# Kernel tuning notes

Measured on AMD Instinct MI355X. Metric: run time of the kernel, lower is better.

Reference implementation:

```python
import jax, jax.numpy as jnp
import numpy as np

D_MODEL = 2048
NUM_HEADS = 16
NUM_KV_HEADS = 4
HEAD_DIM = D_MODEL // NUM_HEADS  # 128
ROPE_THETA = 10000.0
BATCH = 2
SEQ = 2048


def _rotate_half(x):
    # interleaved rotate-half: pairs (x0,x1) -> (-x1, x0)
    x1 = x[..., ::2]
    x2 = x[..., 1::2]
    return jnp.stack((-x2, x1), axis=-1).reshape(x.shape)


def _rope_tables(seq_len, dtype, start_pos=0):
    inv_freq = 1.0 / (ROPE_THETA ** (jnp.arange(0, HEAD_DIM, 2, dtype=jnp.float32) / HEAD_DIM))
    positions = jnp.arange(start_pos, start_pos + seq_len, dtype=jnp.float32)
    freqs = jnp.outer(positions, inv_freq)              # [S, HD/2]
    emb = jnp.repeat(freqs, 2, axis=-1)                  # [S, HD]
    cos = jnp.cos(emb).astype(dtype)[None, None, :, :]   # [1,1,S,HD]
    sin = jnp.sin(emb).astype(dtype)[None, None, :, :]
    return cos, sin


def setup_inputs() -> dict:
    key = jax.random.key(0)
    ks = jax.random.split(key, 5)
    s = 0.02
    x = jax.random.normal(ks[0], (BATCH, SEQ, D_MODEL), dtype=jnp.float32)
    wq = jax.random.normal(ks[1], (D_MODEL, NUM_HEADS * HEAD_DIM), dtype=jnp.float32) * s
    wk = jax.random.normal(ks[2], (D_MODEL, NUM_KV_HEADS * HEAD_DIM), dtype=jnp.float32) * s
    wv = jax.random.normal(ks[3], (D_MODEL, NUM_KV_HEADS * HEAD_DIM), dtype=jnp.float32) * s
    wo = jax.random.normal(ks[4], (D_MODEL, D_MODEL), dtype=jnp.float32) * s
    return {"x": x, "wq": wq, "wk": wk, "wv": wv, "wo": wo}


def reference(x, wq, wk, wv, wo):
    batch, seq_len, _ = x.shape
    # projections (bias-free linears)
    q = (x @ wq).reshape(batch, seq_len, NUM_HEADS, HEAD_DIM).transpose(0, 2, 1, 3)
    k = (x @ wk).reshape(batch, seq_len, NUM_KV_HEADS, HEAD_DIM).transpose(0, 2, 1, 3)
    v = (x @ wv).reshape(batch, seq_len, NUM_KV_HEADS, HEAD_DIM).transpose(0, 2, 1, 3)
    # RoPE
    cos, sin = _rope_tables(seq_len, q.dtype)
    q = q * cos + _rotate_half(q) * sin
    k = k * cos + _rotate_half(k) * sin
    # GQA: duplicate KV heads
    repeats = NUM_HEADS // NUM_KV_HEADS
    k = jnp.repeat(k, repeats, axis=1)
    v = jnp.repeat(v, repeats, axis=1)
    # causal SDPA
    scale = HEAD_DIM ** -0.5
    scores = jnp.einsum('bhqd,bhkd->bhqk', q, k) * scale
    causal = jnp.tril(jnp.ones((seq_len, seq_len), dtype=bool))
    scores = jnp.where(causal[None, None, :, :], scores, -jnp.inf)
    weights = jax.nn.softmax(scores, axis=-1)
    y = jnp.einsum('bhqk,bhkd->bhqd', weights, v)
    y = y.transpose(0, 2, 1, 3).reshape(batch, seq_len, NUM_HEADS * HEAD_DIM)
    return y @ wo
```

## Files before the change

### kernel.cpp

```cpp
#include <hip/hip_runtime.h>
#include <cstdint>
#include <cstddef>

using short8 = __attribute__((ext_vector_type(8))) short;
using f32x4  = __attribute__((ext_vector_type(4))) float;
using u16x4  = __attribute__((ext_vector_type(4))) unsigned short;

#define DEV __device__ __forceinline__

DEV unsigned short f2bf(float f) {
  unsigned int u = __builtin_bit_cast(unsigned int, f);
  u += 0x7fffu + ((u >> 16) & 1u);
  return (unsigned short)(u >> 16);
}
DEV float bf2f(unsigned short h) {
  unsigned int u = ((unsigned int)h) << 16;
  return __builtin_bit_cast(float, u);
}
DEV unsigned int cvtpk_bf16(float lo, float hi) {
  unsigned int d;
  asm("v_cvt_pk_bf16_f32 %0, %1, %2" : "=v"(d) : "v"(lo), "v"(hi));
  return d;
}

#define GLL16(gp, lp)                                                          \
  __builtin_amdgcn_global_load_lds(                                            \
      (const __attribute__((address_space(1))) char*)(const char*)(gp),        \
      (__attribute__((address_space(3))) char*)(char*)(lp), 16, 0, 0)

constexpr int BATCH = 2, SEQ = 2048, DMODEL = 2048, NH = 16, NKVH = 4, DH = 128;
constexpr int MROWS = BATCH * SEQ;
constexpr int NQKV  = DMODEL + 2 * NKVH * DH;
constexpr int KOFF  = DMODEL;
constexpr int VOFF  = DMODEL + NKVH * DH;
constexpr float SM_L2 = 0.12751388158f;


__global__ void k_tables(float* __restrict__ tc, float* __restrict__ ts) {
  int id = blockIdx.x * 256 + threadIdx.x;
  int pos = id >> 6, i = id & 63;
  float freq = __expf(-(float)i * 0.14391157f);
  float ang = (float)pos * freq;
  tc[id] = cosf(ang);
  ts[id] = sinf(ang);
}

__global__ void k_castx(const float* __restrict__ x, unsigned short* __restrict__ xb) {
  int id = blockIdx.x * 256 + threadIdx.x;
  float4 v = ((const float4*)x)[id];
  u16x4 o = { f2bf(v.x), f2bf(v.y), f2bf(v.z), f2bf(v.w) };
  ((u16x4*)xb)[id] = o;
}

__global__ __launch_bounds__(256) void k_wtrans(const float* __restrict__ src,
                                                unsigned short* __restrict__ dst, int N) {
  __shared__ float tile[32][33];
  int n0 = blockIdx.x * 32, k0 = blockIdx.y * 32;
  int tx = threadIdx.x, ty = threadIdx.y;
  #pragma unroll
  for (int r = ty; r < 32; r += 8)
    tile[r][tx] = src[(size_t)(k0 + r) * N + n0 + tx];
  __syncthreads();
  #pragma unroll
  for (int r = ty; r < 32; r += 8)
    dst[(size_t)(n0 + r) * 2048 + k0 + tx] = f2bf(tile[tx][r]);
}

__global__ __launch_bounds__(256) void k_vtrans(const unsigned short* __restrict__ qkv,
                                                unsigned short* __restrict__ vt) {
  __shared__ unsigned short tile[32][33];
  int s0 = blockIdx.x * 32, d0 = blockIdx.y * 32;
  int bk = blockIdx.z;
  const unsigned short* src = qkv + (size_t)(bk >> 2) * SEQ * NQKV + VOFF + (bk & 3) * DH;
  unsigned short* dst = vt + ((size_t)bk * DH + d0) * SEQ + s0;
  int tx = threadIdx.x, ty = threadIdx.y;
  #pragma unroll
  for (int r = ty; r < 32; r += 8)
    tile[r][tx] = src[(size_t)(s0 + r) * NQKV + d0 + tx];
  __syncthreads();
  #pragma unroll
  for (int r = ty; r < 32; r += 8)
    dst[(size_t)r * SEQ + tx] = tile[tx][r];
}


constexpr int BM = 128, BN = 128, BK = 32;

template <bool OUTF32>
__global__ __launch_bounds__(256) void k_gemm_bt(
    const unsigned short* __restrict__ A,
    const unsigned short* __restrict__ Bt,
    void* __restrict__ C, int M, int N, int K) {
  __shared__ unsigned short As[BM * BK];
  __shared__ unsigned short Bs[BN * BK];
  const int t = threadIdx.x;
  const int l = t & 63, w = t >> 6;
  const int wm = w >> 1, wn = w & 1;
  const int gx = gridDim.x;
  const int nwg = gx * gridDim.y;
  const int idl = blockIdx.y * gx + blockIdx.x;
  const int swz = (idl & 7) * (nwg >> 3) + (idl >> 3);
  const int m0 = (swz / gx) * BM, n0 = (swz % gx) * BN;
  const int rl = l & 15, kg = l >> 4;

  f32x4 acc[4][4] = {};

  const int sr = t >> 2;
  const int gq = (t & 3) ^ (sr & 3);
  const unsigned short* aP0 = A  + (size_t)(m0 + sr) * K + gq * 8;
  const unsigned short* aP1 = A  + (size_t)(m0 + 64 + sr) * K + gq * 8;
  const unsigned short* bP0 = Bt + (size_t)(n0 + sr) * K + gq * 8;
  const unsigned short* bP1 = Bt + (size_t)(n0 + 64 + sr) * K + gq * 8;
  char* ldsA = (char*)As;
  char* ldsB = (char*)Bs;
  const int wb = w * 1024;

  const int nk = K / BK;
  for (int kt = 0; kt < nk; ++kt) {
    const int ko = kt * BK;
    __syncthreads();
    GLL16(aP0 + ko, ldsA + wb);
    GLL16(aP1 + ko, ldsA + 4096 + wb);
    GLL16(bP0 + ko, ldsB + wb);
    GLL16(bP1 + ko, ldsB + 4096 + wb);
    __syncthreads();
    short8 aF[4], bF[4];
    #pragma unroll
    for (int mi = 0; mi < 4; ++mi) {
      int r = wm * 64 + mi * 16 + rl;
      aF[mi] = *(const short8*)(ldsA + r * 64 + ((kg ^ (r & 3)) * 16));
    }
    #pragma unroll
    for (int ni = 0; ni < 4; ++ni) {
      int r = wn * 64 + ni * 16 + rl;
      bF[ni] = *(const short8*)(ldsB + r * 64 + ((kg ^ (r & 3)) * 16));
    }
    #pragma unroll
    for (int mi = 0; mi < 4; ++mi)
      #pragma unroll
      for (int ni = 0; ni < 4; ++ni)
        acc[mi][ni] = __builtin_amdgcn_mfma_f32_16x16x32_bf16(aF[mi], bF[ni], acc[mi][ni], 0, 0, 0);
  }

  #pragma unroll
  for (int mi = 0; mi < 4; ++mi) {
    #pragma unroll
    for (int ni = 0; ni < 4; ++ni) {
      int row = m0 + wm * 64 + mi * 16 + kg * 4;
      int col = n0 + wn * 64 + ni * 16 + rl;
      #pragma unroll
      for (int r = 0; r < 4; ++r) {
        if constexpr (OUTF32)
          ((float*)C)[(size_t)(row + r) * N + col] = acc[mi][ni][r];
        else
          ((unsigned short*)C)[(size_t)(row + r) * N + col] = f2bf(acc[mi][ni][r]);
      }
    }
  }
}


__global__ void k_rope(unsigned short* __restrict__ qkv,
                       const float* __restrict__ tc, const float* __restrict__ ts) {
  int id = blockIdx.x * 256 + threadIdx.x;
  int row = id / 1280, p = id % 1280;
  int col, d;
  bool isq = (p < 1024);
  if (isq) { col = 2 * p;               d = p & 63; }
  else     { int pk = p - 1024; col = KOFF + 2 * pk; d = pk & 63; }
  int s = row & (SEQ - 1);
  float c = tc[s * 64 + d], sn = ts[s * 64 + d];
  unsigned int* pp = (unsigned int*)(qkv + (size_t)row * NQKV + col);
  unsigned int v = *pp;
  float x0 = bf2f((unsigned short)(v & 0xffffu));
  float x1 = bf2f((unsigned short)(v >> 16));
  float y0 = x0 * c - x1 * sn;
  float y1 = x1 * c + x0 * sn;
  if (isq) { y0 *= SM_L2; y1 *= SM_L2; }
  *pp = (unsigned int)f2bf(y0) | ((unsigned int)f2bf(y1) << 16);
}


constexpr int QB = 128, KB = 64;
constexpr float THR = 8.0f;

__global__ __launch_bounds__(512, 8) void k_attn(const unsigned short* __restrict__ qkv,
                                                 const unsigned short* __restrict__ vt,
                                                 unsigned short* __restrict__ obuf) {
  __shared__ unsigned short Ks[KB * DH];
  __shared__ unsigned short Vs[DH * KB];
  __shared__ unsigned short Pw[8][16 * 72];

  const int t = threadIdx.x, l = t & 63, w = t >> 6;
  const int rl = l & 15, kg = l >> 4;

  const int id = blockIdx.x;
  const int b = id >> 8;
  const int u = id & 255;
  const int h = u >> 4;
  const int qtr = u & 15;
  const int qt = b ? (15 - qtr) : qtr;
  const int q0 = qt * QB;
  const int kvh = h >> 2;

  const unsigned short* qbase = qkv + (size_t)b * SEQ * NQKV;
  const unsigned short* kbase = qbase + KOFF + kvh * DH;
  const unsigned short* vtb = vt + (size_t)(b * NKVH + kvh) * DH * SEQ;

  const unsigned short* kp[2];
  const unsigned short* vp[2];
  #pragma unroll
  for (int i = 0; i < 2; ++i) {
    int c = i * 512 + t;
    int krow = c >> 4, kq = c & 15;
    kp[i] = kbase + (size_t)krow * NQKV + ((kq ^ (krow & 7)) << 3);
    int vrow = c >> 3, vq = c & 7;
    vp[i] = vtb + (size_t)vrow * SEQ + ((vq ^ (vrow & 7)) << 3);
  }

  const int qw0 = q0 + w * 16;

  short8 qF[4];
  {
    const size_t qr = (size_t)(qw0 + rl) * NQKV + h * DH;
    #pragma unroll
    for (int ks = 0; ks < 4; ++ks)
      qF[ks] = *(const short8*)(qbase + qr + ks * 32 + kg * 8);
  }

  f32x4 Oc[8] = {};
  float mr = -3e38f, lr = 0.f;

  unsigned short* pw = Pw[w];

  for (int kv0 = 0; kv0 < q0 + QB; kv0 += KB) {
    __syncthreads();
    #pragma unroll
    for (int i = 0; i < 2; ++i) {
      GLL16(kp[i] + (size_t)kv0 * NQKV, (char*)Ks + w * 1024 + i * 8192);
      GLL16(vp[i] + kv0,               (char*)Vs + w * 1024 + i * 8192);
    }
    __syncthreads();
    if (kv0 >= qw0 + 16) continue;

    f32x4 St[4] = {};
    __builtin_amdgcn_s_setprio(1);
    #pragma unroll
    for (int n = 0; n < 4; ++n) {
      const int krow = n * 16 + rl;
      #pragma unroll
      for (int ks = 0; ks < 4; ++ks) {
        short8 kF = *(const short8*)&Ks[krow * DH + (((ks * 4 + kg) ^ (rl & 7)) << 3)];
        St[n] = __builtin_amdgcn_mfma_f32_16x16x32_bf16(kF, qF[ks], St[n], 0, 0, 0);
      }
    }
    __builtin_amdgcn_s_setprio(0);

    float mx = -3e38f;
    const bool diag = (kv0 + KB - 1) > qw0;
    if (diag) {
      const int thr = qw0 + rl - kv0;
      #pragma unroll
      for (int n = 0; n < 4; ++n)
        #pragma unroll
        for (int r = 0; r < 4; ++r) {
          float s = St[n][r];
          if (n * 16 + kg * 4 + r > thr) s = -3e38f;
          St[n][r] = s;
          mx = fmaxf(mx, s);
        }
    } else {
      #pragma unroll
      for (int n = 0; n < 4; ++n)
        #pragma unroll
        for (int r = 0; r < 4; ++r) mx = fmaxf(mx, St[n][r]);
    }
    mx = fmaxf(mx, __shfl_xor(mx, 16));
    mx = fmaxf(mx, __shfl_xor(mx, 32));

    const bool need = mx > mr + THR;
    if (__any(need)) {
      const float mnew = fmaxf(mr, mx);
      const float sf = exp2f(mr - mnew);
      mr = mnew;
      lr *= sf;
      float sfv[4];
      #pragma unroll
      for (int r = 0; r < 4; ++r) sfv[r] = __shfl(sf, kg * 4 + r, 16);
      #pragma unroll
      for (int c = 0; c < 8; ++c)
        #pragma unroll
        for (int r = 0; r < 4; ++r) Oc[c][r] *= sfv[r];
    }

    float rs = 0.f;
    #pragma unroll
    for (int n = 0; n < 4; ++n) {
      float e0 = exp2f(St[n][0] - mr);
      float e1 = exp2f(St[n][1] - mr);
      float e2 = exp2f(St[n][2] - mr);
      float e3 = exp2f(St[n][3] - mr);
      rs += (e0 + e1) + (e2 + e3);
      uint2 d;
      d.x = cvtpk_bf16(e0, e1);
      d.y = cvtpk_bf16(e2, e3);
      *(uint2*)&pw[rl * 72 + n * 16 + kg * 4] = d;
    }
    rs += __shfl_xor(rs, 16);
    rs += __shfl_xor(rs, 32);
    lr += rs;

    short8 pF[2];
    #pragma unroll
    for (int ks2 = 0; ks2 < 2; ++ks2)
      pF[ks2] = *(const short8*)&pw[rl * 72 + ks2 * 32 + kg * 8];
    __builtin_amdgcn_s_setprio(1);
    #pragma unroll
    for (int c = 0; c < 8; ++c) {
      const int vrow = c * 16 + rl;
      #pragma unroll
      for (int ks2 = 0; ks2 < 2; ++ks2) {
        short8 vF = *(const short8*)&Vs[vrow * KB + (((ks2 * 4 + kg) ^ (rl & 7)) << 3)];
        Oc[c] = __builtin_amdgcn_mfma_f32_16x16x32_bf16(pF[ks2], vF, Oc[c], 0, 0, 0);
      }
    }
    __builtin_amdgcn_s_setprio(0);
  }

  const float linv = 1.0f / lr;
  float inv[4];
  #pragma unroll
  for (int r = 0; r < 4; ++r) inv[r] = __shfl(linv, kg * 4 + r, 16);
  #pragma unroll
  for (int c = 0; c < 8; ++c)
    #pragma unroll
    for (int r = 0; r < 4; ++r) {
      int row = b * SEQ + qw0 + kg * 4 + r;
      obuf[(size_t)row * DMODEL + h * DH + c * 16 + rl] = f2bf(Oc[c][r] * inv[r]);
    }
}


extern "C" void kernel_launch(void* const* d_in, const int* in_sizes, int n_in,
                              void* d_out, int out_size, void* d_ws, size_t ws_size,
                              hipStream_t stream) {
  const float* x  = (const float*)d_in[0];
  const float* wq = (const float*)d_in[1];
  const float* wk = (const float*)d_in[2];
  const float* wv = (const float*)d_in[3];
  const float* wo = (const float*)d_in[4];
  float* out = (float*)d_out;

  unsigned short* xb  = (unsigned short*)d_ws;
  unsigned short* wT  = xb  + (size_t)MROWS * DMODEL;
  unsigned short* woT = wT  + (size_t)NQKV * DMODEL;
  unsigned short* qkv = woT + (size_t)DMODEL * DMODEL;
  unsigned short* ob  = qkv + (size_t)MROWS * NQKV;
  float* tc = (float*)(ob + (size_t)MROWS * DMODEL);
  float* ts = tc + SEQ * 64;
  unsigned short* vtG = wT;

  k_tables<<<dim3(SEQ * 64 / 256), dim3(256), 0, stream>>>(tc, ts);
  k_castx<<<dim3(MROWS * DMODEL / 4 / 256), dim3(256), 0, stream>>>(x, xb);
  k_wtrans<<<dim3(DMODEL / 32, 64), dim3(32, 8), 0, stream>>>(wq, wT, DMODEL);
  k_wtrans<<<dim3(NKVH * DH / 32, 64), dim3(32, 8), 0, stream>>>(wk, wT + (size_t)DMODEL * 2048, NKVH * DH);
  k_wtrans<<<dim3(NKVH * DH / 32, 64), dim3(32, 8), 0, stream>>>(wv, wT + (size_t)VOFF * 2048, NKVH * DH);
  k_wtrans<<<dim3(DMODEL / 32, 64), dim3(32, 8), 0, stream>>>(wo, woT, DMODEL);

  k_gemm_bt<false><<<dim3(NQKV / BN, MROWS / BM), dim3(256), 0, stream>>>(
      xb, wT, qkv, MROWS, NQKV, DMODEL);
  k_rope<<<dim3(MROWS * 1280 / 256), dim3(256), 0, stream>>>(qkv, tc, ts);
  k_vtrans<<<dim3(SEQ / 32, DH / 32, BATCH * NKVH), dim3(32, 8), 0, stream>>>(qkv, vtG);
  k_attn<<<dim3(512), dim3(512), 0, stream>>>(qkv, vtG, ob);
  k_gemm_bt<true><<<dim3(DMODEL / BN, MROWS / BM), dim3(256), 0, stream>>>(
      ob, woT, out, MROWS, DMODEL, DMODEL);
}
```

Before: 245.8 us.

## Fuse RoPE into QKV GEMM epilogue and double-buffer attention KV tiles

Removes the standalone RoPE kernel by applying rotation and Q scaling in the QKV GEMM epilogue via lane shuffles, saving a read/write pass over Q and K. The attention kernel halves the KV tile to 32 and double-buffers K/V in shared memory with async loads and explicit vmcnt waits so the next tile loads while the current one computes. This adds more loop iterations and barriers, and RoPE now runs on fp32 accumulators before bf16 rounding.

```diff
diff --git a/kernel.cpp b/kernel.cpp
--- a/kernel.cpp
+++ b/kernel.cpp
@@ -86,11 +86,12 @@
 
 constexpr int BM = 128, BN = 128, BK = 32;
 
-template <bool OUTF32>
+template <bool OUTF32, bool ROPE>
 __global__ __launch_bounds__(256) void k_gemm_bt(
     const unsigned short* __restrict__ A,
     const unsigned short* __restrict__ Bt,
-    void* __restrict__ C, int M, int N, int K) {
+    void* __restrict__ C, int M, int N, int K,
+    const float* __restrict__ tc, const float* __restrict__ ts) {
   __shared__ unsigned short As[BM * BK];
   __shared__ unsigned short Bs[BN * BK];
   const int t = threadIdx.x;
@@ -146,50 +147,45 @@
   for (int mi = 0; mi < 4; ++mi) {
     #pragma unroll
     for (int ni = 0; ni < 4; ++ni) {
-      int row = m0 + wm * 64 + mi * 16 + kg * 4;
-      int col = n0 + wn * 64 + ni * 16 + rl;
+      const int row0 = m0 + wm * 64 + mi * 16 + kg * 4;
+      const int colb = n0 + wn * 64 + ni * 16;
+      const int col = colb + rl;
+      if constexpr (ROPE) {
+        if (colb < VOFF) {
+          const int dd = (col & 127) >> 1;
+          const float sgn = (col & 1) ? 1.0f : -1.0f;
+          const float qs = (colb < KOFF) ? SM_L2 : 1.0f;
+          #pragma unroll
+          for (int r = 0; r < 4; ++r) {
+            const int s = (row0 + r) & (SEQ - 1);
+            const float c = tc[s * 64 + dd], sn = ts[s * 64 + dd];
+            const float xv = acc[mi][ni][r];
+            const float xp = __shfl_xor(xv, 1);
+            acc[mi][ni][r] = (xv * c + sgn * xp * sn) * qs;
+          }
+        }
+      }
       #pragma unroll
       for (int r = 0; r < 4; ++r) {
         if constexpr (OUTF32)
-          ((float*)C)[(size_t)(row + r) * N + col] = acc[mi][ni][r];
+          ((float*)C)[(size_t)(row0 + r) * N + col] = acc[mi][ni][r];
         else
-          ((unsigned short*)C)[(size_t)(row + r) * N + col] = f2bf(acc[mi][ni][r]);
+          ((unsigned short*)C)[(size_t)(row0 + r) * N + col] = f2bf(acc[mi][ni][r]);
       }
     }
   }
 }
 
 
-__global__ void k_rope(unsigned short* __restrict__ qkv,
-                       const float* __restrict__ tc, const float* __restrict__ ts) {
-  int id = blockIdx.x * 256 + threadIdx.x;
-  int row = id / 1280, p = id % 1280;
-  int col, d;
-  bool isq = (p < 1024);
-  if (isq) { col = 2 * p;               d = p & 63; }
-  else     { int pk = p - 1024; col = KOFF + 2 * pk; d = pk & 63; }
-  int s = row & (SEQ - 1);
-  float c = tc[s * 64 + d], sn = ts[s * 64 + d];
-  unsigned int* pp = (unsigned int*)(qkv + (size_t)row * NQKV + col);
-  unsigned int v = *pp;
-  float x0 = bf2f((unsigned short)(v & 0xffffu));
-  float x1 = bf2f((unsigned short)(v >> 16));
-  float y0 = x0 * c - x1 * sn;
-  float y1 = x1 * c + x0 * sn;
-  if (isq) { y0 *= SM_L2; y1 *= SM_L2; }
-  *pp = (unsigned int)f2bf(y0) | ((unsigned int)f2bf(y1) << 16);
-}
-
-
-constexpr int QB = 128, KB = 64;
+constexpr int QB = 128, KB = 32;
 constexpr float THR = 8.0f;
 
 __global__ __launch_bounds__(512, 8) void k_attn(const unsigned short* __restrict__ qkv,
                                                  const unsigned short* __restrict__ vt,
                                                  unsigned short* __restrict__ obuf) {
-  __shared__ unsigned short Ks[KB * DH];
-  __shared__ unsigned short Vs[DH * KB];
-  __shared__ unsigned short Pw[8][16 * 72];
+  __shared__ unsigned short Ks[2][KB * DH];
+  __shared__ unsigned short Vs[2][DH * KB];
+  __shared__ unsigned short Pw[8][16 * 40];
 
   const int t = threadIdx.x, l = t & 63, w = t >> 6;
   const int rl = l & 15, kg = l >> 4;
@@ -207,16 +203,10 @@
   const unsigned short* kbase = qbase + KOFF + kvh * DH;
   const unsigned short* vtb = vt + (size_t)(b * NKVH + kvh) * DH * SEQ;
 
-  const unsigned short* kp[2];
-  const unsigned short* vp[2];
-  #pragma unroll
-  for (int i = 0; i < 2; ++i) {
-    int c = i * 512 + t;
-    int krow = c >> 4, kq = c & 15;
-    kp[i] = kbase + (size_t)krow * NQKV + ((kq ^ (krow & 7)) << 3);
-    int vrow = c >> 3, vq = c & 7;
-    vp[i] = vtb + (size_t)vrow * SEQ + ((vq ^ (vrow & 7)) << 3);
-  }
+  const int krow = t >> 4, kq = t & 15;
+  const int vrow = t >> 2, vq = t & 3;
+  const unsigned short* kp = kbase + (size_t)krow * NQKV + ((kq ^ (krow & 7)) << 3);
+  const unsigned short* vp = vtb + (size_t)vrow * SEQ + ((vq ^ (vrow & 3)) << 3);
 
   const int qw0 = q0 + w * 16;
 
@@ -232,99 +222,108 @@
   float mr = -3e38f, lr = 0.f;
 
   unsigned short* pw = Pw[w];
-
-  for (int kv0 = 0; kv0 < q0 + QB; kv0 += KB) {
-    __syncthreads();
-    #pragma unroll
-    for (int i = 0; i < 2; ++i) {
-      GLL16(kp[i] + (size_t)kv0 * NQKV, (char*)Ks + w * 1024 + i * 8192);
-      GLL16(vp[i] + kv0,               (char*)Vs + w * 1024 + i * 8192);
-    }
-    __syncthreads();
-    if (kv0 >= qw0 + 16) continue;
-
-    f32x4 St[4] = {};
-    __builtin_amdgcn_s_setprio(1);
-    #pragma unroll
-    for (int n = 0; n < 4; ++n) {
-      const int krow = n * 16 + rl;
-      #pragma unroll
-      for (int ks = 0; ks < 4; ++ks) {
-        short8 kF = *(const short8*)&Ks[krow * DH + (((ks * 4 + kg) ^ (rl & 7)) << 3)];
-        St[n] = __builtin_amdgcn_mfma_f32_16x16x32_bf16(kF, qF[ks], St[n], 0, 0, 0);
-      }
-    }
-    __builtin_amdgcn_s_setprio(0);
-
-    float mx = -3e38f;
-    const bool diag = (kv0 + KB - 1) > qw0;
-    if (diag) {
-      const int thr = qw0 + rl - kv0;
-      #pragma unroll
-      for (int n = 0; n < 4; ++n)
-        #pragma unroll
-        for (int r = 0; r < 4; ++r) {
-          float s = St[n][r];
-          if (n * 16 + kg * 4 + r > thr) s = -3e38f;
-          St[n][r] = s;
-          mx = fmaxf(mx, s);
+  const int nt = q0 / KB + 4;
+
+  GLL16(kp, (char*)Ks[0] + w * 1024);
+  GLL16(vp, (char*)Vs[0] + w * 1024);
+
+  int cur = 0;
+  for (int tt = 0; tt < nt; ++tt) {
+    const int kv0 = tt * KB;
+    const bool more = (tt + 1 < nt);
+    if (more) {
+      GLL16(kp + (size_t)(kv0 + KB) * NQKV, (char*)Ks[cur ^ 1] + w * 1024);
+      GLL16(vp + (kv0 + KB),               (char*)Vs[cur ^ 1] + w * 1024);
+      asm volatile("s_waitcnt vmcnt(2)" ::: "memory");
+    } else {
+      asm volatile("s_waitcnt vmcnt(0)" ::: "memory");
+    }
+    __builtin_amdgcn_sched_barrier(0);
+    __builtin_amdgcn_s_barrier();
+
+    if (kv0 < qw0 + 16) {
+      const unsigned short* KsC = Ks[cur];
+      const unsigned short* VsC = Vs[cur];
+
+      f32x4 St[2] = {};
+      __builtin_amdgcn_s_setprio(1);
+      #pragma unroll
+      for (int n = 0; n < 2; ++n) {
+        const int kr = n * 16 + rl;
+        #pragma unroll
+        for (int ks = 0; ks < 4; ++ks) {
+          short8 kF = *(const short8*)&KsC[kr * DH + (((ks * 4 + kg) ^ (kr & 7)) << 3)];
+          St[n] = __builtin_amdgcn_mfma_f32_16x16x32_bf16(kF, qF[ks], St[n], 0, 0, 0);
         }
-    } else {
-      #pragma unroll
-      for (int n = 0; n < 4; ++n)
-        #pragma unroll
-        for (int r = 0; r < 4; ++r) mx = fmaxf(mx, St[n][r]);
-    }
-    mx = fmaxf(mx, __shfl_xor(mx, 16));
-    mx = fmaxf(mx, __shfl_xor(mx, 32));
-
-    const bool need = mx > mr + THR;
-    if (__any(need)) {
-      const float mnew = fmaxf(mr, mx);
-      const float sf = exp2f(mr - mnew);
-      mr = mnew;
-      lr *= sf;
-      float sfv[4];
-      #pragma unroll
-      for (int r = 0; r < 4; ++r) sfv[r] = __shfl(sf, kg * 4 + r, 16);
-      #pragma unroll
-      for (int c = 0; c < 8; ++c)
-        #pragma unroll
-        for (int r = 0; r < 4; ++r) Oc[c][r] *= sfv[r];
-    }
-
-    float rs = 0.f;
-    #pragma unroll
-    for (int n = 0; n < 4; ++n) {
-      float e0 = exp2f(St[n][0] - mr);
-      float e1 = exp2f(St[n][1] - mr);
-      float e2 = exp2f(St[n][2] - mr);
-      float e3 = exp2f(St[n][3] - mr);
-      rs += (e0 + e1) + (e2 + e3);
-      uint2 d;
-      d.x = cvtpk_bf16(e0, e1);
-      d.y = cvtpk_bf16(e2, e3);
-      *(uint2*)&pw[rl * 72 + n * 16 + kg * 4] = d;
-    }
-    rs += __shfl_xor(rs, 16);
-    rs += __shfl_xor(rs, 32);
-    lr += rs;
-
-    short8 pF[2];
-    #pragma unroll
-    for (int ks2 = 0; ks2 < 2; ++ks2)
-      pF[ks2] = *(const short8*)&pw[rl * 72 + ks2 * 32 + kg * 8];
-    __builtin_amdgcn_s_setprio(1);
-    #pragma unroll
-    for (int c = 0; c < 8; ++c) {
-      const int vrow = c * 16 + rl;
-      #pragma unroll
-      for (int ks2 = 0; ks2 < 2; ++ks2) {
-        short8 vF = *(const short8*)&Vs[vrow * KB + (((ks2 * 4 + kg) ^ (rl & 7)) << 3)];
-        Oc[c] = __builtin_amdgcn_mfma_f32_16x16x32_bf16(pF[ks2], vF, Oc[c], 0, 0, 0);
-      }
-    }
-    __builtin_amdgcn_s_setprio(0);
+      }
+      __builtin_amdgcn_s_setprio(0);
+
+      float mx = -3e38f;
+      const bool diag = (kv0 + KB - 1) > qw0;
+      if (diag) {
+        const int thr = qw0 + rl - kv0;
+        #pragma unroll
+        for (int n = 0; n < 2; ++n)
+          #pragma unroll
+          for (int r = 0; r < 4; ++r) {
+            float s = St[n][r];
+            if (n * 16 + kg * 4 + r > thr) s = -3e38f;
+            St[n][r] = s;
+            mx = fmaxf(mx, s);
+          }
+      } else {
+        #pragma unroll
+        for (int n = 0; n < 2; ++n)
+          #pragma unroll
+          for (int r = 0; r < 4; ++r) mx = fmaxf(mx, St[n][r]);
+      }
+      mx = fmaxf(mx, __shfl_xor(mx, 16));
+      mx = fmaxf(mx, __shfl_xor(mx, 32));
+
+      if (__any(mx > mr + THR)) {
+        const float mnew = fmaxf(mr, mx);
+        const float sf = exp2f(mr - mnew);
+        mr = mnew;
+        lr *= sf;
+        float sfv[4];
+        #pragma unroll
+        for (int r = 0; r < 4; ++r) sfv[r] = __shfl(sf, kg * 4 + r, 16);
+        #pragma unroll
+        for (int c = 0; c < 8; ++c)
+          #pragma unroll
+          for (int r = 0; r < 4; ++r) Oc[c][r] *= sfv[r];
+      }
+
+      float rs = 0.f;
+      #pragma unroll
+      for (int n = 0; n < 2; ++n) {
+        float e0 = exp2f(St[n][0] - mr);
+        float e1 = exp2f(St[n][1] - mr);
+        float e2 = exp2f(St[n][2] - mr);
+        float e3 = exp2f(St[n][3] - mr);
+        rs += (e0 + e1) + (e2 + e3);
+        uint2 d;
+        d.x = cvtpk_bf16(e0, e1);
+        d.y = cvtpk_bf16(e2, e3);
+        *(uint2*)&pw[rl * 40 + n * 16 + kg * 4] = d;
+      }
+      rs += __shfl_xor(rs, 16);
+      rs += __shfl_xor(rs, 32);
+      lr += rs;
+
+      short8 pFv = *(const short8*)&pw[rl * 40 + kg * 8];
+      __builtin_amdgcn_s_setprio(1);
+      #pragma unroll
+      for (int c = 0; c < 8; ++c) {
+        const int vr = c * 16 + rl;
+        short8 vF = *(const short8*)&VsC[vr * KB + ((kg ^ (vr & 3)) << 3)];
+        Oc[c] = __builtin_amdgcn_mfma_f32_16x16x32_bf16(pFv, vF, Oc[c], 0, 0, 0);
+      }
+      __builtin_amdgcn_s_setprio(0);
+    }
+
+    __builtin_amdgcn_s_barrier();
+    cur ^= 1;
   }
 
   const float linv = 1.0f / lr;
@@ -367,11 +366,10 @@
   k_wtrans<<<dim3(NKVH * DH / 32, 64), dim3(32, 8), 0, stream>>>(wv, wT + (size_t)VOFF * 2048, NKVH * DH);
   k_wtrans<<<dim3(DMODEL / 32, 64), dim3(32, 8), 0, stream>>>(wo, woT, DMODEL);
 
-  k_gemm_bt<false><<<dim3(NQKV / BN, MROWS / BM), dim3(256), 0, stream>>>(
-      xb, wT, qkv, MROWS, NQKV, DMODEL);
-  k_rope<<<dim3(MROWS * 1280 / 256), dim3(256), 0, stream>>>(qkv, tc, ts);
+  k_gemm_bt<false, true><<<dim3(NQKV / BN, MROWS / BM), dim3(256), 0, stream>>>(
+      xb, wT, qkv, MROWS, NQKV, DMODEL, tc, ts);
   k_vtrans<<<dim3(SEQ / 32, DH / 32, BATCH * NKVH), dim3(32, 8), 0, stream>>>(qkv, vtG);
   k_attn<<<dim3(512), dim3(512), 0, stream>>>(qkv, vtG, ob);
-  k_gemm_bt<true><<<dim3(DMODEL / BN, MROWS / BM), dim3(256), 0, stream>>>(
-      ob, woT, out, MROWS, DMODEL, DMODEL);
-}
+  k_gemm_bt<true, false><<<dim3(DMODEL / BN, MROWS / BM), dim3(256), 0, stream>>>(
+      ob, woT, out, MROWS, DMODEL, DMODEL, nullptr, nullptr);
+}
```

Result: slower. 260.6 us (+6.0%).
